# Kernel tuning notes

Hardware: AMD Instinct MI355X
Metric: run time of the kernel (lower is better)

Reference implementation:

```python
import jax, jax.numpy as jnp
import numpy as np

B, S, D = 2, 2048, 640
H, DH = 8, 80  # heads, dim_head
SCALE = DH ** -0.5


def setup_inputs() -> dict:
    key = jax.random.key(0)
    ks = jax.random.split(key, 7)
    std = D ** -0.5
    return {
        "x": jax.random.normal(ks[0], (B, S, D), jnp.float32),
        "encoder_hidden_states": jax.random.normal(ks[1], (B, S, D), jnp.float32),
        # Linear weights stored as [in, out] so application is x @ W
        "Wq": jax.random.normal(ks[2], (D, H * DH), jnp.float32) * std,
        "Wk": jax.random.normal(ks[3], (D, H * DH), jnp.float32) * std,
        "Wv": jax.random.normal(ks[4], (D, H * DH), jnp.float32) * std,
        "Wo": jax.random.normal(ks[5], (H * DH, D), jnp.float32) * std,
        "bo": jax.random.normal(ks[6], (D,), jnp.float32) * 0.01,
    }


def reference(x, encoder_hidden_states, Wq, Wk, Wv, Wo, bo):
    # projections (to_q/to_k/to_v have bias=False)
    q = x @ Wq                      # [B, S, H*DH]
    k = encoder_hidden_states @ Wk  # [B, S, H*DH]
    v = encoder_hidden_states @ Wv  # [B, S, H*DH]

    def split_heads(t):
        b, s, _ = t.shape
        return t.reshape(b, s, H, DH).transpose(0, 2, 1, 3)  # [B, H, S, DH]

    q, k, v = split_heads(q), split_heads(k), split_heads(v)

    # the torch loop over bh-chunks computes plain softmax attention; same math fused
    scores = jnp.einsum("bhid,bhjd->bhij", q, k) * SCALE  # [B, H, Sq, Skv]
    attn = jax.nn.softmax(scores, axis=-1)
    out = jnp.einsum("bhij,bhjd->bhid", attn, v)          # [B, H, Sq, DH]

    out = out.transpose(0, 2, 1, 3).reshape(x.shape[0], x.shape[1], H * DH)
    return out @ Wo + bo  # to_out[0]; Dropout(p=0) is identity
```

## Files before the change

### kernel.cpp

```cpp
#include <hip/hip_runtime.h>
#include <hip/hip_bf16.h>

typedef __bf16 v4bf __attribute__((ext_vector_type(4)));
typedef __bf16 v8bf __attribute__((ext_vector_type(8)));
typedef float  v4f  __attribute__((ext_vector_type(4)));

namespace {
constexpr int Bb  = 2;
constexpr int Ss  = 2048;
constexpr int Dd  = 640;
constexpr int Hh  = 8;
constexpr int DHh = 80;
constexpr int Mm  = Bb * Ss;
constexpr float kQScale = 0.11180339887498949f * 1.4426950408889634f;

__device__ __forceinline__ float4 ld4(const float* p) {
  return *reinterpret_cast<const float4*>(p);
}

__device__ __forceinline__ v8bf pack8(float4 f0, float4 f1) {
  v8bf p;
  p[0]=(__bf16)f0.x; p[1]=(__bf16)f0.y; p[2]=(__bf16)f0.z; p[3]=(__bf16)f0.w;
  p[4]=(__bf16)f1.x; p[5]=(__bf16)f1.y; p[6]=(__bf16)f1.z; p[7]=(__bf16)f1.w;
  return p;
}

__device__ __forceinline__ float exp2_hw(float x) {
  float r;
  asm("v_exp_f32 %0, %1" : "=v"(r) : "v"(x));
  return r;
}
}

__global__ __launch_bounds__(256)
void wtrans_kernel(const float* __restrict__ Wq, const float* __restrict__ Wk,
                   const float* __restrict__ Wv, const float* __restrict__ Wo,
                   __bf16* __restrict__ Wtq, __bf16* __restrict__ Wtk,
                   __bf16* __restrict__ Wtv, __bf16* __restrict__ Wto) {
  const int z = blockIdx.z;
  const float* W = (z == 0) ? Wq : (z == 1) ? Wk : (z == 2) ? Wv : Wo;
  __bf16* Wt = (z == 0) ? Wtq : (z == 1) ? Wtk : (z == 2) ? Wtv : Wto;
  const int k0 = blockIdx.y * 32, n0 = blockIdx.x * 32;
  __shared__ float t[32][33];
  const int tid = threadIdx.x;
  {
    int kr = tid >> 3, c4 = (tid & 7) * 4;
    float4 f = ld4(W + (size_t)(k0 + kr) * Dd + n0 + c4);
    t[kr][c4 + 0] = f.x; t[kr][c4 + 1] = f.y;
    t[kr][c4 + 2] = f.z; t[kr][c4 + 3] = f.w;
  }
  __syncthreads();
  {
    int nr = tid >> 3, kc = (tid & 7) * 4;
    v4bf p;
#pragma unroll
    for (int u = 0; u < 4; ++u) p[u] = (__bf16)t[kc + u][nr];
    *reinterpret_cast<v4bf*>(&Wt[(size_t)(n0 + nr) * Dd + k0 + kc]) = p;
  }
}

template <bool AF32>
__device__ __forceinline__ void gemm_core_db(const void* __restrict__ Ap,
                                             const __bf16* __restrict__ Bt,
                                             __bf16* As, __bf16* Bs, int m0,
                                             int n0, int rh, int ch,
                                             v4f acc[4][4]) {
  constexpr int BUF = 128 * 40;
  constexpr int NKB = Dd / 32;
  const int tid = threadIdx.x;
  const int lane = tid & 63;
  const int quad = lane >> 4, l15 = lane & 15;
  const int lr = tid >> 1;
  const int lk = (tid & 1) * 16;
  const __bf16* Bg = Bt + (size_t)(n0 + lr) * Dd + lk;
  const float* Af = (const float*)Ap;
  const __bf16* Ab = (const __bf16*)Ap;

#pragma unroll
  for (int i = 0; i < 4; ++i)
#pragma unroll
    for (int j = 0; j < 4; ++j) acc[i][j] = (v4f){0.f, 0.f, 0.f, 0.f};

  v8bf a0, a1, b0, b1;
  if constexpr (AF32) {
    const float* ap = Af + (size_t)(m0 + lr) * Dd + lk;
    a0 = pack8(ld4(ap), ld4(ap + 4));
    a1 = pack8(ld4(ap + 8), ld4(ap + 12));
  } else {
    const __bf16* ap = Ab + (size_t)(m0 + lr) * Dd + lk;
    a0 = *reinterpret_cast<const v8bf*>(ap);
    a1 = *reinterpret_cast<const v8bf*>(ap + 8);
  }
  b0 = *reinterpret_cast<const v8bf*>(Bg);
  b1 = *reinterpret_cast<const v8bf*>(Bg + 8);
  *reinterpret_cast<v8bf*>(&As[lr * 40 + lk])     = a0;
  *reinterpret_cast<v8bf*>(&As[lr * 40 + lk + 8]) = a1;
  *reinterpret_cast<v8bf*>(&Bs[lr * 40 + lk])     = b0;
  *reinterpret_cast<v8bf*>(&Bs[lr * 40 + lk + 8]) = b1;

  for (int it = 0; it < NKB; ++it) {
    if (it + 1 < NKB) {
      const int kb = (it + 1) * 32;
      if constexpr (AF32) {
        const float* ap = Af + (size_t)(m0 + lr) * Dd + kb + lk;
        a0 = pack8(ld4(ap), ld4(ap + 4));
        a1 = pack8(ld4(ap + 8), ld4(ap + 12));
      } else {
        const __bf16* ap = Ab + (size_t)(m0 + lr) * Dd + kb + lk;
        a0 = *reinterpret_cast<const v8bf*>(ap);
        a1 = *reinterpret_cast<const v8bf*>(ap + 8);
      }
      b0 = *reinterpret_cast<const v8bf*>(Bg + kb);
      b1 = *reinterpret_cast<const v8bf*>(Bg + kb + 8);
    }
    __syncthreads();
    const int cur = (it & 1) * BUF, nxt = BUF - cur;
    v8bf af[4], bv[4];
#pragma unroll
    for (int i = 0; i < 4; ++i)
      af[i] = *reinterpret_cast<const v8bf*>(
          &As[cur + (rh + i * 16 + l15) * 40 + quad * 8]);
#pragma unroll
    for (int j = 0; j < 4; ++j)
      bv[j] = *reinterpret_cast<const v8bf*>(
          &Bs[cur + (ch + j * 16 + l15) * 40 + quad * 8]);
#pragma unroll
    for (int i = 0; i < 4; ++i)
#pragma unroll
      for (int j = 0; j < 4; ++j)
        acc[i][j] = __builtin_amdgcn_mfma_f32_16x16x32_bf16(af[i], bv[j],
                                                            acc[i][j], 0, 0, 0);
    if (it + 1 < NKB) {
      *reinterpret_cast<v8bf*>(&As[nxt + lr * 40 + lk])     = a0;
      *reinterpret_cast<v8bf*>(&As[nxt + lr * 40 + lk + 8]) = a1;
      *reinterpret_cast<v8bf*>(&Bs[nxt + lr * 40 + lk])     = b0;
      *reinterpret_cast<v8bf*>(&Bs[nxt + lr * 40 + lk + 8]) = b1;
    }
  }
}

__global__ __launch_bounds__(256)
void gemm_qkv_mfma(const float* __restrict__ x, const float* __restrict__ ehs,
                   const __bf16* __restrict__ Wtq,
                   const __bf16* __restrict__ Wtk,
                   const __bf16* __restrict__ Wtv, __bf16* __restrict__ qb,
                   __bf16* __restrict__ kbuf, __bf16* __restrict__ vb) {
  const int z = blockIdx.z;
  const float* A = (z == 0) ? x : ehs;
  const __bf16* Bt = (z == 0) ? Wtq : (z == 1) ? Wtk : Wtv;
  __bf16* C = (z == 0) ? qb : (z == 1) ? kbuf : vb;
  const float scale = (z == 0) ? kQScale : 1.0f;

  __shared__ __bf16 As[2 * 128 * 40];
  __shared__ __bf16 Bs[2 * 128 * 40];
  const int tid = threadIdx.x;
  const int w = tid >> 6, lane = tid & 63;
  const int quad = lane >> 4, l15 = lane & 15;
  const int m0 = blockIdx.y * 128, n0 = blockIdx.x * 128;
  const int rh = (w >> 1) * 64, ch = (w & 1) * 64;
  v4f acc[4][4];
  gemm_core_db<true>(A, Bt, As, Bs, m0, n0, rh, ch, acc);

  if (z == 2) {
#pragma unroll
    for (int i = 0; i < 4; ++i)
#pragma unroll
      for (int j = 0; j < 4; ++j) {
        int m = m0 + rh + i * 16 + quad * 4;
        int n = n0 + ch + j * 16 + l15;
        int bb = m >> 11, tok = m & 2047;
        v4bf pk;
#pragma unroll
        for (int r = 0; r < 4; ++r) pk[r] = (__bf16)acc[i][j][r];
        *reinterpret_cast<v4bf*>(&C[((size_t)bb * Dd + n) * Ss + tok]) = pk;
      }
  } else {
#pragma unroll
    for (int i = 0; i < 4; ++i)
#pragma unroll
      for (int j = 0; j < 4; ++j) {
        int m = m0 + rh + i * 16 + quad * 4;
        int n = n0 + ch + j * 16 + l15;
        int hh = n / DHh, d = n % DHh;
        int bb = m >> 11, tok = m & 2047;
        __bf16* base = &C[(((size_t)bb * Hh + hh) * Ss + tok) * DHh + d];
#pragma unroll
        for (int r = 0; r < 4; ++r)
          base[(size_t)r * DHh] = (__bf16)(acc[i][j][r] * scale);
      }
  }
}

__global__ __launch_bounds__(256)
void gemm_out_mfma(const __bf16* __restrict__ A, const __bf16* __restrict__ Bt,
                   const float* __restrict__ bias, float* __restrict__ out) {
  __shared__ __bf16 As[2 * 128 * 40];
  __shared__ __bf16 Bs[2 * 128 * 40];
  const int tid = threadIdx.x;
  const int w = tid >> 6, lane = tid & 63;
  const int quad = lane >> 4, l15 = lane & 15;
  const int m0 = blockIdx.y * 128, n0 = blockIdx.x * 128;
  const int rh = (w >> 1) * 64, ch = (w & 1) * 64;
  v4f acc[4][4];
  gemm_core_db<false>(A, Bt, As, Bs, m0, n0, rh, ch, acc);

#pragma unroll
  for (int i = 0; i < 4; ++i)
#pragma unroll
    for (int j = 0; j < 4; ++j) {
      int m = m0 + rh + i * 16 + quad * 4;
      int n = n0 + ch + j * 16 + l15;
      float bn = bias[n];
#pragma unroll
      for (int r = 0; r < 4; ++r)
        out[(size_t)(m + r) * Dd + n] = acc[i][j][r] + bn;
    }
}

__global__ __launch_bounds__(256, 2)
void attn_mfma_kernel(const __bf16* __restrict__ q,
                      const __bf16* __restrict__ k,
                      const __bf16* __restrict__ vtg, __bf16* __restrict__ o) {
  constexpr int QT = 64;
  constexpr int KT = 32;
  constexpr int KW = Ss / 4;
  constexpr int NIT = KW / KT;
  constexpr int LQ = 104;
  constexpr int LV = 40;
  constexpr int KS = KT * LQ;
  constexpr int VS = 96 * LV;
  constexpr int PS = QT * LV;
  constexpr int WSZ = KS + VS + PS;
  constexpr int LM = 100;

  __shared__ __align__(16) __bf16 smem[4 * WSZ];

  const int bh = blockIdx.x;
  const int b = bh >> 3, h = bh & 7;
  const int q0 = blockIdx.y * QT;
  const int tid = threadIdx.x;
  const int w = tid >> 6;
  const int lane = tid & 63;
  const int quad = lane >> 4;
  const int l15 = lane & 15;

  __bf16* ksw = smem + w * WSZ;
  __bf16* vtw = ksw + KS;
  __bf16* psw = vtw + VS;

  const __bf16* qg  = q + ((size_t)(b * Hh + h) * Ss + q0) * DHh;
  const __bf16* kgb = k + (size_t)(b * Hh + h) * Ss * DHh;
  const __bf16* vgb = vtg + ((size_t)b * Dd + h * DHh) * Ss;

  v8bf qf[4][3];
#pragma unroll
  for (int qt = 0; qt < 4; ++qt)
#pragma unroll
    for (int s = 0; s < 3; ++s) {
      if (s == 2 && quad >= 2) {
        qf[qt][s] = (v8bf){};
      } else {
        qf[qt][s] = *reinterpret_cast<const v8bf*>(
            qg + (size_t)(qt * 16 + l15) * DHh + s * 32 + quad * 8);
      }
    }

  int klr[5];
#pragma unroll
  for (int c = 0; c < 5; ++c) {
    int E = c * 512 + lane * 8;
    klr[c] = (E / DHh) * LQ + (E % DHh);
  }
  const int vgo = (lane >> 2) * Ss + (lane & 3) * 8;
  const int vlo = (lane >> 2) * LV + (lane & 3) * 8;

  {
    v8bf z8 = {};
    *reinterpret_cast<v8bf*>(&ksw[(lane >> 1) * LQ + 80 + (lane & 1) * 8]) = z8;
    v8bf pad = {};
    int vr = 80 + (lane >> 2);
    if (vr == 80) {
#pragma unroll
      for (int e = 0; e < 8; ++e) pad[e] = (__bf16)1.f;
    }
    *reinterpret_cast<v8bf*>(&vtw[vr * LV + (lane & 3) * 8]) = pad;
  }
  {
    const __bf16* kg = kgb + (size_t)(w * KW) * DHh;
#pragma unroll
    for (int c = 0; c < 5; ++c)
      *reinterpret_cast<v8bf*>(&ksw[klr[c]]) =
          *reinterpret_cast<const v8bf*>(kg + c * 512 + lane * 8);
  }

  v4f Oacc[4][6];
#pragma unroll
  for (int qt = 0; qt < 4; ++qt)
#pragma unroll
    for (int mt = 0; mt < 6; ++mt) Oacc[qt][mt] = (v4f){0.f, 0.f, 0.f, 0.f};

  for (int it = 0; it < NIT; ++it) {
    const bool pfK = (it + 1 < NIT);
    v8bf kreg[5];
    if (pfK) {
      const __bf16* kg = kgb + (size_t)(w * KW + (it + 1) * KT) * DHh;
#pragma unroll
      for (int c = 0; c < 5; ++c)
        kreg[c] = *reinterpret_cast<const v8bf*>(kg + c * 512 + lane * 8);
    }

    v4f sacc[4][2];
#pragma unroll
    for (int qt = 0; qt < 4; ++qt) {
      sacc[qt][0] = (v4f){0.f, 0.f, 0.f, 0.f};
      sacc[qt][1] = (v4f){0.f, 0.f, 0.f, 0.f};
    }
    __builtin_amdgcn_s_setprio(1);
#pragma unroll
    for (int s = 0; s < 3; ++s) {
      v8bf ak0 = *reinterpret_cast<const v8bf*>(
          &ksw[l15 * LQ + s * 32 + quad * 8]);
      v8bf ak1 = *reinterpret_cast<const v8bf*>(
          &ksw[(16 + l15) * LQ + s * 32 + quad * 8]);
#pragma unroll
      for (int qt = 0; qt < 4; ++qt) {
        sacc[qt][0] = __builtin_amdgcn_mfma_f32_16x16x32_bf16(
            ak0, qf[qt][s], sacc[qt][0], 0, 0, 0);
        sacc[qt][1] = __builtin_amdgcn_mfma_f32_16x16x32_bf16(
            ak1, qf[qt][s], sacc[qt][1], 0, 0, 0);
      }
    }

    v8bf vreg[5];
    {
      const __bf16* vg = vgb + (w * KW + it * KT);
#pragma unroll
      for (int c = 0; c < 5; ++c)
        vreg[c] = *reinterpret_cast<const v8bf*>(vg + vgo +
                                                 (size_t)c * 16 * Ss);
    }

    if (it > 0) {
      v8bf bp[4];
#pragma unroll
      for (int qt = 0; qt < 4; ++qt)
        bp[qt] = *reinterpret_cast<const v8bf*>(
            &psw[(qt * 16 + l15) * LV + quad * 8]);
#pragma unroll
      for (int mt = 0; mt < 6; ++mt) {
        v8bf av = *reinterpret_cast<const v8bf*>(
            &vtw[(mt * 16 + l15) * LV + quad * 8]);
#pragma unroll
        for (int qt = 0; qt < 4; ++qt)
          Oacc[qt][mt] = __builtin_amdgcn_mfma_f32_16x16x32_bf16(
              av, bp[qt], Oacc[qt][mt], 0, 0, 0);
      }
    }
    __builtin_amdgcn_s_setprio(0);

#pragma unroll
    for (int qt = 0; qt < 4; ++qt)
#pragma unroll
      for (int mt = 0; mt < 2; ++mt) {
        v4bf pk;
#pragma unroll
        for (int r = 0; r < 4; ++r)
          pk[r] = (__bf16)exp2_hw(sacc[qt][mt][r]);
        *reinterpret_cast<v4bf*>(
            &psw[(qt * 16 + l15) * LV + mt * 16 + quad * 4]) = pk;
      }

    if (pfK) {
#pragma unroll
      for (int c = 0; c < 5; ++c)
        *reinterpret_cast<v8bf*>(&ksw[klr[c]]) = kreg[c];
    }
#pragma unroll
    for (int c = 0; c < 5; ++c)
      *reinterpret_cast<v8bf*>(&vtw[vlo + c * 16 * LV]) = vreg[c];
  }

  {
    v8bf bp[4];
#pragma unroll
    for (int qt = 0; qt < 4; ++qt)
      bp[qt] = *reinterpret_cast<const v8bf*>(
          &psw[(qt * 16 + l15) * LV + quad * 8]);
    __builtin_amdgcn_s_setprio(1);
#pragma unroll
    for (int mt = 0; mt < 6; ++mt) {
      v8bf av = *reinterpret_cast<const v8bf*>(
          &vtw[(mt * 16 + l15) * LV + quad * 8]);
#pragma unroll
      for (int qt = 0; qt < 4; ++qt)
        Oacc[qt][mt] = __builtin_amdgcn_mfma_f32_16x16x32_bf16(
            av, bp[qt], Oacc[qt][mt], 0, 0, 0);
    }
    __builtin_amdgcn_s_setprio(0);
  }

  __syncthreads();
  float* mrg = (float*)smem;
  if (w >= 2) {
    float* base = mrg + (w - 2) * (QT * LM);
#pragma unroll
    for (int qt = 0; qt < 4; ++qt)
#pragma unroll
      for (int mt = 0; mt < 6; ++mt)
        *reinterpret_cast<v4f*>(
            &base[(qt * 16 + l15) * LM + mt * 16 + quad * 4]) = Oacc[qt][mt];
  }
  __syncthreads();
  if (w < 2) {
    const float* base = mrg + w * (QT * LM);
#pragma unroll
    for (int qt = 0; qt < 4; ++qt)
#pragma unroll
      for (int mt = 0; mt < 6; ++mt)
        Oacc[qt][mt] += *reinterpret_cast<const v4f*>(
            &base[(qt * 16 + l15) * LM + mt * 16 + quad * 4]);
  }
  __syncthreads();
  if (w == 1) {
#pragma unroll
    for (int qt = 0; qt < 4; ++qt)
#pragma unroll
      for (int mt = 0; mt < 6; ++mt)
        *reinterpret_cast<v4f*>(
            &mrg[(qt * 16 + l15) * LM + mt * 16 + quad * 4]) = Oacc[qt][mt];
  }
  __syncthreads();
  if (w == 0) {
#pragma unroll
    for (int qt = 0; qt < 4; ++qt)
#pragma unroll
      for (int mt = 0; mt < 6; ++mt)
        Oacc[qt][mt] += *reinterpret_cast<const v4f*>(
            &mrg[(qt * 16 + l15) * LM + mt * 16 + quad * 4]);
#pragma unroll
    for (int qt = 0; qt < 4; ++qt) {
      float lsum = __shfl(Oacc[qt][5][0], l15);
      float inv = 1.f / lsum;
      __bf16* og =
          o + (size_t)(b * Ss + q0 + qt * 16 + l15) * Dd + h * DHh;
#pragma unroll
      for (int mt = 0; mt < 5; ++mt) {
        v4bf pk;
#pragma unroll
        for (int r = 0; r < 4; ++r) pk[r] = (__bf16)(Oacc[qt][mt][r] * inv);
        *reinterpret_cast<v4bf*>(&og[mt * 16 + quad * 4]) = pk;
      }
    }
  }
}

extern "C" void kernel_launch(void* const* d_in, const int* in_sizes, int n_in,
                              void* d_out, int out_size, void* d_ws,
                              size_t ws_size, hipStream_t stream) {
  const float* x   = (const float*)d_in[0];
  const float* ehs = (const float*)d_in[1];
  const float* Wq  = (const float*)d_in[2];
  const float* Wk  = (const float*)d_in[3];
  const float* Wv  = (const float*)d_in[4];
  const float* Wo  = (const float*)d_in[5];
  const float* bo  = (const float*)d_in[6];
  float* out = (float*)d_out;

  __bf16* qb  = (__bf16*)d_ws;
  __bf16* kb  = qb + (size_t)Mm * Dd;
  __bf16* vb  = kb + (size_t)Mm * Dd;
  __bf16* ab  = vb + (size_t)Mm * Dd;
  __bf16* Wtq = ab + (size_t)Mm * Dd;
  __bf16* Wtk = Wtq + (size_t)Dd * Dd;
  __bf16* Wtv = Wtk + (size_t)Dd * Dd;
  __bf16* Wto = Wtv + (size_t)Dd * Dd;

  wtrans_kernel<<<dim3(Dd / 32, Dd / 32, 4), 256, 0, stream>>>(
      Wq, Wk, Wv, Wo, Wtq, Wtk, Wtv, Wto);
  gemm_qkv_mfma<<<dim3(Dd / 128, Mm / 128, 3), 256, 0, stream>>>(
      x, ehs, Wtq, Wtk, Wtv, qb, kb, vb);
  attn_mfma_kernel<<<dim3(Bb * Hh, Ss / 64), 256, 0, stream>>>(qb, kb, vb, ab);
  gemm_out_mfma<<<dim3(Dd / 128, Mm / 128), 256, 0, stream>>>(ab, Wto, bo,
                                                              out);
}
```

Baseline: 150.1 us.

## Tile V into per-head 32-token blocks and shrink output GEMM tile

The QKV GEMM now writes V transposed into contiguous [b,h,token-block,d,32] tiles, so each attention wave loads its V chunk as contiguous 512-element runs instead of strided rows across the sequence. The output projection gets its own kernel with 128x64 tiles, which doubles the block count to give more parallelism across CUs. The price is less reuse per block in the output GEMM, and the V store pattern in the QKV epilogue changes.

```diff
diff --git a/kernel.cpp b/kernel.cpp
--- a/kernel.cpp
+++ b/kernel.cpp
@@ -59,8 +59,7 @@
   }
 }
 
-template <bool AF32>
-__device__ __forceinline__ void gemm_core_db(const void* __restrict__ Ap,
+__device__ __forceinline__ void gemm_core_db(const float* __restrict__ Af,
                                              const __bf16* __restrict__ Bt,
                                              __bf16* As, __bf16* Bs, int m0,
                                              int n0, int rh, int ch,
@@ -73,8 +72,6 @@
   const int lr = tid >> 1;
   const int lk = (tid & 1) * 16;
   const __bf16* Bg = Bt + (size_t)(n0 + lr) * Dd + lk;
-  const float* Af = (const float*)Ap;
-  const __bf16* Ab = (const __bf16*)Ap;
 
 #pragma unroll
   for (int i = 0; i < 4; ++i)
@@ -82,14 +79,10 @@
     for (int j = 0; j < 4; ++j) acc[i][j] = (v4f){0.f, 0.f, 0.f, 0.f};
 
   v8bf a0, a1, b0, b1;
-  if constexpr (AF32) {
+  {
     const float* ap = Af + (size_t)(m0 + lr) * Dd + lk;
     a0 = pack8(ld4(ap), ld4(ap + 4));
     a1 = pack8(ld4(ap + 8), ld4(ap + 12));
-  } else {
-    const __bf16* ap = Ab + (size_t)(m0 + lr) * Dd + lk;
-    a0 = *reinterpret_cast<const v8bf*>(ap);
-    a1 = *reinterpret_cast<const v8bf*>(ap + 8);
   }
   b0 = *reinterpret_cast<const v8bf*>(Bg);
   b1 = *reinterpret_cast<const v8bf*>(Bg + 8);
@@ -101,15 +94,9 @@
   for (int it = 0; it < NKB; ++it) {
     if (it + 1 < NKB) {
       const int kb = (it + 1) * 32;
-      if constexpr (AF32) {
-        const float* ap = Af + (size_t)(m0 + lr) * Dd + kb + lk;
-        a0 = pack8(ld4(ap), ld4(ap + 4));
-        a1 = pack8(ld4(ap + 8), ld4(ap + 12));
-      } else {
-        const __bf16* ap = Ab + (size_t)(m0 + lr) * Dd + kb + lk;
-        a0 = *reinterpret_cast<const v8bf*>(ap);
-        a1 = *reinterpret_cast<const v8bf*>(ap + 8);
-      }
+      const float* ap = Af + (size_t)(m0 + lr) * Dd + kb + lk;
+      a0 = pack8(ld4(ap), ld4(ap + 4));
+      a1 = pack8(ld4(ap + 8), ld4(ap + 12));
       b0 = *reinterpret_cast<const v8bf*>(Bg + kb);
       b1 = *reinterpret_cast<const v8bf*>(Bg + kb + 8);
     }
@@ -159,7 +146,7 @@
   const int m0 = blockIdx.y * 128, n0 = blockIdx.x * 128;
   const int rh = (w >> 1) * 64, ch = (w & 1) * 64;
   v4f acc[4][4];
-  gemm_core_db<true>(A, Bt, As, Bs, m0, n0, rh, ch, acc);
+  gemm_core_db(A, Bt, As, Bs, m0, n0, rh, ch, acc);
 
   if (z == 2) {
 #pragma unroll
@@ -168,11 +155,15 @@
       for (int j = 0; j < 4; ++j) {
         int m = m0 + rh + i * 16 + quad * 4;
         int n = n0 + ch + j * 16 + l15;
+        int hh = n / DHh, d = n % DHh;
         int bb = m >> 11, tok = m & 2047;
+        int tb = tok >> 5, t = tok & 31;
         v4bf pk;
 #pragma unroll
         for (int r = 0; r < 4; ++r) pk[r] = (__bf16)acc[i][j][r];
-        *reinterpret_cast<v4bf*>(&C[((size_t)bb * Dd + n) * Ss + tok]) = pk;
+        *reinterpret_cast<v4bf*>(
+            &C[((((size_t)bb * Hh + hh) * (Ss / 32) + tb) * DHh + d) * 32 +
+               t]) = pk;
       }
   } else {
 #pragma unroll
@@ -194,20 +185,70 @@
 __global__ __launch_bounds__(256)
 void gemm_out_mfma(const __bf16* __restrict__ A, const __bf16* __restrict__ Bt,
                    const float* __restrict__ bias, float* __restrict__ out) {
-  __shared__ __bf16 As[2 * 128 * 40];
-  __shared__ __bf16 Bs[2 * 128 * 40];
+  constexpr int BUFA = 128 * 40, BUFB = 64 * 40;
+  constexpr int NKB = Dd / 32;
+  __shared__ __bf16 As[2 * BUFA];
+  __shared__ __bf16 Bs[2 * BUFB];
   const int tid = threadIdx.x;
   const int w = tid >> 6, lane = tid & 63;
   const int quad = lane >> 4, l15 = lane & 15;
-  const int m0 = blockIdx.y * 128, n0 = blockIdx.x * 128;
-  const int rh = (w >> 1) * 64, ch = (w & 1) * 64;
-  v4f acc[4][4];
-  gemm_core_db<false>(A, Bt, As, Bs, m0, n0, rh, ch, acc);
-
+  const int m0 = blockIdx.y * 128, n0 = blockIdx.x * 64;
+  const int rh = (w >> 1) * 64, ch = (w & 1) * 32;
+  const int lrA = tid >> 1, lkA = (tid & 1) * 16;
+  const int lrB = tid >> 2, lkB = (tid & 3) * 8;
+  const __bf16* Ag = A + (size_t)(m0 + lrA) * Dd + lkA;
+  const __bf16* Bg = Bt + (size_t)(n0 + lrB) * Dd + lkB;
+
+  v4f acc[4][2];
 #pragma unroll
   for (int i = 0; i < 4; ++i)
 #pragma unroll
-    for (int j = 0; j < 4; ++j) {
+    for (int j = 0; j < 2; ++j) acc[i][j] = (v4f){0.f, 0.f, 0.f, 0.f};
+
+  v8bf a0, a1, b0;
+  a0 = *reinterpret_cast<const v8bf*>(Ag);
+  a1 = *reinterpret_cast<const v8bf*>(Ag + 8);
+  b0 = *reinterpret_cast<const v8bf*>(Bg);
+  *reinterpret_cast<v8bf*>(&As[lrA * 40 + lkA])     = a0;
+  *reinterpret_cast<v8bf*>(&As[lrA * 40 + lkA + 8]) = a1;
+  *reinterpret_cast<v8bf*>(&Bs[lrB * 40 + lkB])     = b0;
+
+  for (int it = 0; it < NKB; ++it) {
+    if (it + 1 < NKB) {
+      const int kb = (it + 1) * 32;
+      a0 = *reinterpret_cast<const v8bf*>(Ag + kb);
+      a1 = *reinterpret_cast<const v8bf*>(Ag + kb + 8);
+      b0 = *reinterpret_cast<const v8bf*>(Bg + kb);
+    }
+    __syncthreads();
+    const int curA = (it & 1) * BUFA, nxtA = BUFA - curA;
+    const int curB = (it & 1) * BUFB, nxtB = BUFB - curB;
+    v8bf af[4], bv[2];
+#pragma unroll
+    for (int i = 0; i < 4; ++i)
+      af[i] = *reinterpret_cast<const v8bf*>(
+          &As[curA + (rh + i * 16 + l15) * 40 + quad * 8]);
+#pragma unroll
+    for (int j = 0; j < 2; ++j)
+      bv[j] = *reinterpret_cast<const v8bf*>(
+          &Bs[curB + (ch + j * 16 + l15) * 40 + quad * 8]);
+#pragma unroll
+    for (int i = 0; i < 4; ++i)
+#pragma unroll
+      for (int j = 0; j < 2; ++j)
+        acc[i][j] = __builtin_amdgcn_mfma_f32_16x16x32_bf16(af[i], bv[j],
+                                                            acc[i][j], 0, 0, 0);
+    if (it + 1 < NKB) {
+      *reinterpret_cast<v8bf*>(&As[nxtA + lrA * 40 + lkA])     = a0;
+      *reinterpret_cast<v8bf*>(&As[nxtA + lrA * 40 + lkA + 8]) = a1;
+      *reinterpret_cast<v8bf*>(&Bs[nxtB + lrB * 40 + lkB])     = b0;
+    }
+  }
+
+#pragma unroll
+  for (int i = 0; i < 4; ++i)
+#pragma unroll
+    for (int j = 0; j < 2; ++j) {
       int m = m0 + rh + i * 16 + quad * 4;
       int n = n0 + ch + j * 16 + l15;
       float bn = bias[n];
@@ -250,7 +291,7 @@
 
   const __bf16* qg  = q + ((size_t)(b * Hh + h) * Ss + q0) * DHh;
   const __bf16* kgb = k + (size_t)(b * Hh + h) * Ss * DHh;
-  const __bf16* vgb = vtg + ((size_t)b * Dd + h * DHh) * Ss;
+  const __bf16* vgb = vtg + (size_t)(b * Hh + h) * Ss * DHh;
 
   v8bf qf[4][3];
 #pragma unroll
@@ -271,7 +312,6 @@
     int E = c * 512 + lane * 8;
     klr[c] = (E / DHh) * LQ + (E % DHh);
   }
-  const int vgo = (lane >> 2) * Ss + (lane & 3) * 8;
   const int vlo = (lane >> 2) * LV + (lane & 3) * 8;
 
   {
@@ -333,11 +373,10 @@
 
     v8bf vreg[5];
     {
-      const __bf16* vg = vgb + (w * KW + it * KT);
+      const __bf16* vg = vgb + (size_t)(w * 16 + it) * (KT * DHh);
 #pragma unroll
       for (int c = 0; c < 5; ++c)
-        vreg[c] = *reinterpret_cast<const v8bf*>(vg + vgo +
-                                                 (size_t)c * 16 * Ss);
+        vreg[c] = *reinterpret_cast<const v8bf*>(vg + c * 512 + lane * 8);
     }
 
     if (it > 0) {
@@ -480,6 +519,6 @@
   gemm_qkv_mfma<<<dim3(Dd / 128, Mm / 128, 3), 256, 0, stream>>>(
       x, ehs, Wtq, Wtk, Wtv, qb, kb, vb);
   attn_mfma_kernel<<<dim3(Bb * Hh, Ss / 64), 256, 0, stream>>>(qb, kb, vb, ab);
-  gemm_out_mfma<<<dim3(Dd / 128, Mm / 128), 256, 0, stream>>>(ab, Wto, bo,
-                                                              out);
-}
+  gemm_out_mfma<<<dim3(Dd / 64, Mm / 128), 256, 0, stream>>>(ab, Wto, bo,
+                                                             out);
+}
```

After: 147.8 us. About the same (-1.5%).
